# Kernel optimization log

Hardware: AMD Instinct MI355X
Metric: run time of the kernel (lower is better)

## Reference

```python
import jax, jax.numpy as jnp
import numpy as np

B, T, D = 2, 2048, 1024
H, RANK = 16, 32
DH = D // H  # 64


def setup_inputs() -> dict:
    key = jax.random.key(0)
    ks = jax.random.split(key, 6)
    sd = 1.0 / np.sqrt(D)
    sdh = 1.0 / np.sqrt(DH)
    return {
        "x": jax.random.normal(ks[0], (B, T, D), dtype=jnp.float32),
        "W_qkv": jax.random.normal(ks[1], (D, 3 * D), dtype=jnp.float32) * sd,
        "W_q_lsr": jax.random.normal(ks[2], (H, DH, RANK), dtype=jnp.float32) * sdh,
        "W_k_lsr": jax.random.normal(ks[3], (H, DH, RANK), dtype=jnp.float32) * sdh,
        "lsr_core": jnp.ones((H, RANK), dtype=jnp.float32),
        "W_o": jax.random.normal(ks[4], (D, D), dtype=jnp.float32) * sd,
    }


def reference(x, W_qkv, W_q_lsr, W_k_lsr, lsr_core, W_o):
    b, t, d = x.shape
    # Fused QKV projection
    qkv = x @ W_qkv  # (B, T, 3D)
    q, k, v = jnp.split(qkv, 3, axis=-1)
    # (B, H, T, DH)
    q = q.reshape(b, t, H, DH).transpose(0, 2, 1, 3)
    k = k.reshape(b, t, H, DH).transpose(0, 2, 1, 3)
    v = v.reshape(b, t, H, DH).transpose(0, 2, 1, 3)
    # Low-rank bilinear score: q^T Wq diag(core) Wk^T k
    ql = jnp.einsum("bhtd,hdr->bhtr", q, W_q_lsr)  # (B, H, T, R)
    kl = jnp.einsum("bhsd,hdr->bhsr", k, W_k_lsr)  # (B, H, T, R)
    scale = 1.0 / jnp.sqrt(jnp.asarray(RANK, dtype=x.dtype))
    scores = jnp.einsum("bhtr,bhsr->bhts", ql * lsr_core[None, :, None, :], kl) * scale
    # Causal mask
    causal = jnp.tril(jnp.ones((t, t), dtype=bool))
    scores = jnp.where(causal[None, None], scores, jnp.asarray(-jnp.inf, dtype=scores.dtype))
    attn = jax.nn.softmax(scores, axis=-1)
    y = jnp.einsum("bhts,bhsd->bhtd", attn, v)  # (B, H, T, DH)
    y = y.transpose(0, 2, 1, 3).reshape(b, t, d)
    return y @ W_o
```

## Files before the change

### kernel.cpp

```cpp
#include <hip/hip_runtime.h>
#include <hip/hip_bf16.h>

#define B_  2
#define T_  2048
#define D_  1024
#define H_  16
#define DH_ 64
#define R_  32
#define BT_ (B_*T_)
#define BH_ (B_*H_)

typedef unsigned short u16;
typedef unsigned int   u32;
typedef __attribute__((ext_vector_type(8))) short bhalf8;
typedef __attribute__((ext_vector_type(4))) float floatx4;

#define WSB_FLAG  0
#define WSB_XB    256
#define WSB_WCATT (WSB_XB    + 8388608)
#define WSB_QL    (WSB_WCATT + 4194304)
#define WSB_KL    (WSB_QL    + 4194304)
#define WSB_VT    (WSB_KL    + 4194304)
#define WSB_YB    (WSB_VT    + 8388608)
#define WSB_WOT   (WSB_YB    + 8388608)

#define NEG_ -1.0e30f

__device__ __forceinline__ float bfs(u16 s) {
    union { u32 i; float f; } w; w.i = ((u32)s) << 16; return w.f;
}
__device__ __forceinline__ u16 tob(float f) {
    __hip_bfloat16 h = __float2bfloat16(f);
    return *(u16*)&h;
}
__device__ __forceinline__ u32 pack2(float a, float b) {
    return (u32)tob(a) | ((u32)tob(b) << 16);
}

__global__ __launch_bounds__(64) void detect_dtype(const u32* __restrict__ xw,
                                                   int* __restrict__ flag)
{
    const int tid = threadIdx.x;
    int hits = 0;
    for (int i = tid; i < 512; i += 64) {
        const u32 w = xw[i];
        const u32 h = w & 0xFFFFu;
        const u32 e = (h >> 7) & 0xFFu;
        if (h == 0u || (e >= 100u && e <= 150u)) ++hits;
    }
    #pragma unroll
    for (int off = 32; off; off >>= 1) hits += __shfl_down(hits, off, 64);
    if (tid == 0) *flag = (hits >= 300) ? 1 : 0;
}

__global__ __launch_bounds__(256) void convert_x(
    const void* __restrict__ x, u16* __restrict__ xb,
    const int* __restrict__ flag)
{
    const int isbf = *flag;
    const int e = blockIdx.x * 256 + threadIdx.x;
    if (isbf) {
        ((uint4*)xb)[e] = ((const uint4*)x)[e];
    } else {
        float4 a0 = ((const float4*)x)[2*e];
        float4 a1 = ((const float4*)x)[2*e + 1];
        uint4 o;
        o.x = pack2(a0.x, a0.y); o.y = pack2(a0.z, a0.w);
        o.z = pack2(a1.x, a1.y); o.w = pack2(a1.z, a1.w);
        ((uint4*)xb)[e] = o;
    }
}

__global__ __launch_bounds__(256) void fold_mfma(
    const void* __restrict__ Wqkv, const void* __restrict__ Wq_lsr,
    const void* __restrict__ Wk_lsr, const void* __restrict__ core,
    u16* __restrict__ WcatT, const int* __restrict__ flag)
{
    __shared__ __align__(16) u16 Bq[128 * 72];
    __shared__ __align__(16) u16 Bk[128 * 72];
    __shared__ __align__(16) u16 Aq[32 * 72];
    __shared__ __align__(16) u16 Ak[32 * 72];
    const int isbf = *flag;
    const int tid  = threadIdx.x;
    const int lane = tid & 63;
    const int w    = tid >> 6;
    const int n16  = lane & 15;
    const int q4   = lane >> 4;
    const int h    = blockIdx.y;
    const int d0   = blockIdx.x * 128;

    #pragma unroll
    for (int p = 0; p < 8; ++p) {
        const int e  = tid + p * 256;
        const int r  = e & 31, dh = e >> 5;
        float aq, ak;
        if (isbf) {
            aq = bfs(((const u16*)Wq_lsr)[(h*DH_ + dh)*R_ + r]);
            ak = bfs(((const u16*)Wk_lsr)[(h*DH_ + dh)*R_ + r]);
        } else {
            aq = ((const float*)Wq_lsr)[(h*DH_ + dh)*R_ + r];
            ak = ((const float*)Wk_lsr)[(h*DH_ + dh)*R_ + r];
        }
        Aq[r * 72 + dh] = tob(aq);
        Ak[r * 72 + dh] = tob(ak);
    }
    #pragma unroll
    for (int p = 0; p < 8; ++p) {
        const int e  = tid + p * 256;
        const int n  = e >> 4, ch = e & 15;
        if (isbf) {
            uint2 wq = *(const uint2*)((const u16*)Wqkv + (size_t)(d0+n)*(3*D_) + h*DH_ + ch*4);
            uint2 wk = *(const uint2*)((const u16*)Wqkv + (size_t)(d0+n)*(3*D_) + D_ + h*DH_ + ch*4);
            *(uint2*)&Bq[n * 72 + ch*4] = wq;
            *(uint2*)&Bk[n * 72 + ch*4] = wk;
        } else {
            float4 fq = *(const float4*)((const float*)Wqkv + (size_t)(d0+n)*(3*D_) + h*DH_ + ch*4);
            float4 fk = *(const float4*)((const float*)Wqkv + (size_t)(d0+n)*(3*D_) + D_ + h*DH_ + ch*4);
            uint2 oq, ok;
            oq.x = pack2(fq.x, fq.y); oq.y = pack2(fq.z, fq.w);
            ok.x = pack2(fk.x, fk.y); ok.y = pack2(fk.z, fk.w);
            *(uint2*)&Bq[n * 72 + ch*4] = oq;
            *(uint2*)&Bk[n * 72 + ch*4] = ok;
        }
    }
    __syncthreads();

    floatx4 accq[2][2], acck[2][2];
    #pragma unroll
    for (int mi = 0; mi < 2; ++mi)
        #pragma unroll
        for (int ni = 0; ni < 2; ++ni) { accq[mi][ni] = (floatx4)(0.f); acck[mi][ni] = (floatx4)(0.f); }

    #pragma unroll
    for (int kk = 0; kk < 2; ++kk) {
        bhalf8 aqf[2], akf[2], bqf[2], bkf[2];
        #pragma unroll
        for (int mi = 0; mi < 2; ++mi) {
            aqf[mi] = *(const bhalf8*)&Aq[(mi*16 + n16) * 72 + kk*32 + q4*8];
            akf[mi] = *(const bhalf8*)&Ak[(mi*16 + n16) * 72 + kk*32 + q4*8];
        }
        #pragma unroll
        for (int ni = 0; ni < 2; ++ni) {
            bqf[ni] = *(const bhalf8*)&Bq[(w*32 + ni*16 + n16) * 72 + kk*32 + q4*8];
            bkf[ni] = *(const bhalf8*)&Bk[(w*32 + ni*16 + n16) * 72 + kk*32 + q4*8];
        }
        #pragma unroll
        for (int mi = 0; mi < 2; ++mi)
            #pragma unroll
            for (int ni = 0; ni < 2; ++ni) {
                accq[mi][ni] = __builtin_amdgcn_mfma_f32_16x16x32_bf16(aqf[mi], bqf[ni], accq[mi][ni], 0, 0, 0);
                acck[mi][ni] = __builtin_amdgcn_mfma_f32_16x16x32_bf16(akf[mi], bkf[ni], acck[mi][ni], 0, 0, 0);
            }
    }

    const float scale = 0.17677669529663687f;
    #pragma unroll
    for (int mi = 0; mi < 2; ++mi) {
        #pragma unroll
        for (int rr = 0; rr < 4; ++rr) {
            const int r = mi*16 + q4*4 + rr;
            const float cc = (isbf ? bfs(((const u16*)core)[h*R_ + r])
                                   : ((const float*)core)[h*R_ + r]) * scale;
            #pragma unroll
            for (int ni = 0; ni < 2; ++ni) {
                const int d = d0 + w*32 + ni*16 + n16;
                WcatT[(size_t)(h*R_ + r) * D_ + d]       = tob(accq[mi][ni][rr] * cc);
                WcatT[(size_t)(512 + h*R_ + r) * D_ + d] = tob(acck[mi][ni][rr]);
            }
        }
    }
}

__global__ __launch_bounds__(256) void convert_T(
    const void* __restrict__ src, u16* __restrict__ dst,
    int srcStride, int srcColOff, int dstRowOff, const int* __restrict__ flag)
{
    __shared__ __align__(16) u16 tile[64 * 72];
    const int isbf = *flag;
    const int tid = threadIdx.x;
    const int j0  = blockIdx.x * 64;
    const int i0  = blockIdx.y * 64;
    #pragma unroll
    for (int p = 0; p < 2; ++p) {
        const int e = tid + p * 256;
        const int r = e >> 3, ch = e & 7;
        if (isbf) {
            uint4 w = *(const uint4*)((const u16*)src + (size_t)(i0 + r) * srcStride + srcColOff + j0 + ch*8);
            *(uint4*)&tile[r * 72 + ch*8] = w;
        } else {
            const float* s = (const float*)src + (size_t)(i0 + r) * srcStride + srcColOff + j0 + ch*8;
            float4 a0 = *(const float4*)s;
            float4 a1 = *(const float4*)(s + 4);
            uint4 o;
            o.x = pack2(a0.x, a0.y); o.y = pack2(a0.z, a0.w);
            o.z = pack2(a1.x, a1.y); o.w = pack2(a1.z, a1.w);
            *(uint4*)&tile[r * 72 + ch*8] = o;
        }
    }
    __syncthreads();
    #pragma unroll
    for (int p = 0; p < 2; ++p) {
        const int e = tid + p * 256;
        const int c = e >> 3, ch = e & 7;
        u16 tmp[8];
        #pragma unroll
        for (int j = 0; j < 8; ++j) tmp[j] = tile[(ch*8 + j) * 72 + c];
        *(uint4*)(dst + (size_t)(dstRowOff + j0 + c) * D_ + i0 + ch*8) = *(uint4*)tmp;
    }
}

__global__ __launch_bounds__(256) void gemm1_mfma(
    const u16* __restrict__ xb, const u16* __restrict__ WcatT,
    u16* __restrict__ ql, u16* __restrict__ kl, u16* __restrict__ v_t)
{
    __shared__ __align__(16) u16 As[128 * 72];
    __shared__ __align__(16) u16 Bs[64 * 72];
    const int tid  = threadIdx.x;
    const int lane = tid & 63;
    const int w    = tid >> 6;
    const int n16  = lane & 15;
    const int q4   = lane >> 4;
    const int wx   = w & 1;
    const int wy   = w >> 1;
    const int bm   = blockIdx.y * 128;
    const int bn   = blockIdx.x * 64;

    floatx4 acc[4][2];
    #pragma unroll
    for (int i = 0; i < 4; ++i)
        #pragma unroll
        for (int j = 0; j < 2; ++j) acc[i][j] = (floatx4)(0.f);

    for (int kt = 0; kt < D_; kt += 64) {
        #pragma unroll
        for (int p = 0; p < 4; ++p) {
            const int e = tid + p * 256;
            const int r = e >> 3, ch = (e & 7) * 8;
            *(uint4*)&As[r * 72 + ch] = *(const uint4*)(xb + (size_t)(bm + r) * D_ + kt + ch);
        }
        #pragma unroll
        for (int p = 0; p < 2; ++p) {
            const int e = tid + p * 256;
            const int r = e >> 3, ch = (e & 7) * 8;
            *(uint4*)&Bs[r * 72 + ch] = *(const uint4*)(WcatT + (size_t)(bn + r) * D_ + kt + ch);
        }
        __syncthreads();
        #pragma unroll
        for (int kk = 0; kk < 2; ++kk) {
            bhalf8 a[4], b[2];
            #pragma unroll
            for (int mi = 0; mi < 4; ++mi)
                a[mi] = *(const bhalf8*)&As[(wy*64 + mi*16 + n16) * 72 + kk*32 + q4*8];
            #pragma unroll
            for (int ni = 0; ni < 2; ++ni)
                b[ni] = *(const bhalf8*)&Bs[(wx*32 + ni*16 + n16) * 72 + kk*32 + q4*8];
            #pragma unroll
            for (int mi = 0; mi < 4; ++mi)
                #pragma unroll
                for (int ni = 0; ni < 2; ++ni)
                    acc[mi][ni] = __builtin_amdgcn_mfma_f32_16x16x32_bf16(
                        a[mi], b[ni], acc[mi][ni], 0, 0, 0);
        }
        __syncthreads();
    }

    if (bn < 1024) {
        #pragma unroll
        for (int mi = 0; mi < 4; ++mi) {
            #pragma unroll
            for (int rr = 0; rr < 4; ++rr) {
                const int row = bm + wy*64 + mi*16 + q4*4 + rr;
                const int b   = row >> 11;
                const int t   = row & (T_ - 1);
                #pragma unroll
                for (int ni = 0; ni < 2; ++ni) {
                    const int col = bn + wx*32 + ni*16 + n16;
                    const u16 val = tob(acc[mi][ni][rr]);
                    if (col < 512) {
                        const int h = col >> 5, r = col & 31;
                        ql[((size_t)(b*H_ + h)*T_ + t)*R_ + r] = val;
                    } else {
                        const int c = col - 512; const int h = c >> 5, r = c & 31;
                        kl[((size_t)(b*H_ + h)*T_ + t)*R_ + r] = val;
                    }
                }
            }
        }
    } else {
        #pragma unroll
        for (int mi = 0; mi < 4; ++mi) {
            const int row0 = bm + wy*64 + mi*16 + q4*4;
            const int b = row0 >> 11;
            const int t = row0 & (T_ - 1);
            #pragma unroll
            for (int ni = 0; ni < 2; ++ni) {
                const int c = bn - 1024 + wx*32 + ni*16 + n16;
                const int h = c >> 6, dh = c & 63;
                uint2 o;
                o.x = pack2(acc[mi][ni][0], acc[mi][ni][1]);
                o.y = pack2(acc[mi][ni][2], acc[mi][ni][3]);
                *(uint2*)(v_t + ((size_t)(b*H_ + h) * DH_ + dh) * T_ + t) = o;
            }
        }
    }
}

__global__ __launch_bounds__(256, 2) void attn_kernel(
    const u16* __restrict__ ql, const u16* __restrict__ kl,
    const u16* __restrict__ v_t, u16* __restrict__ y)
{
    __shared__ __align__(16) u16 qls[64 * 40];
    __shared__ __align__(16) u16 kls[128 * 40];
    __shared__ __align__(16) u16 vsT[64 * 136];
    __shared__ __align__(16) u16 Ps [64 * 144];

    const int tid  = threadIdx.x;
    const int lane = tid & 63;
    const int w    = tid >> 6;
    const int n16  = lane & 15;
    const int q4   = lane >> 4;
    const int bh   = blockIdx.x;
    const int qt   = 31 - (int)blockIdx.y;
    const int t0   = qt * 64;
    const int nt   = (qt + 2) >> 1;

    {
        const int r = tid >> 2, ch = tid & 3;
        uint4 x = *(const uint4*)(ql + ((size_t)bh * T_ + t0 + r) * R_ + ch*8);
        *(uint4*)&qls[r * 40 + ch*8] = x;
    }
    bhalf8 aq = *(const bhalf8*)&qls[(w*16 + n16) * 40 + q4*8];

    const u16* klb = kl  + (size_t)bh * T_ * R_;
    const u16* vtb = v_t + (size_t)bh * DH_ * T_;
    const int rk = tid >> 2, ck = (tid & 3) * 8;
    const int dv = tid >> 4, cv = (tid & 15) * 8;

    uint4 kc0 = *(const uint4*)(klb + (size_t)(rk     ) * R_ + ck);
    uint4 kc1 = *(const uint4*)(klb + (size_t)(rk + 64) * R_ + ck);
    uint4 vc0 = *(const uint4*)(vtb + (size_t)(dv     ) * T_ + cv);
    uint4 vc1 = *(const uint4*)(vtb + (size_t)(dv + 16) * T_ + cv);
    uint4 vc2 = *(const uint4*)(vtb + (size_t)(dv + 32) * T_ + cv);
    uint4 vc3 = *(const uint4*)(vtb + (size_t)(dv + 48) * T_ + cv);
    uint4 kn0 = kc0, kn1 = kc1, vn0 = vc0, vn1 = vc1, vn2 = vc2, vn3 = vc3;

    float m[4], l[4];
    floatx4 O[4];
    #pragma unroll
    for (int r = 0; r < 4; ++r) { m[r] = NEG_; l[r] = 0.f; }
    #pragma unroll
    for (int c = 0; c < 4; ++c) O[c] = (floatx4)(0.f);

    for (int it = 0; it < nt; ++it) {
        const int s0 = it * 128;
        __syncthreads();
        *(uint4*)&kls[(rk     ) * 40 + ck] = kc0;
        *(uint4*)&kls[(rk + 64) * 40 + ck] = kc1;
        *(uint4*)&vsT[(dv     ) * 136 + cv] = vc0;
        *(uint4*)&vsT[(dv + 16) * 136 + cv] = vc1;
        *(uint4*)&vsT[(dv + 32) * 136 + cv] = vc2;
        *(uint4*)&vsT[(dv + 48) * 136 + cv] = vc3;
        if (it + 1 < nt) {
            const int s1 = s0 + 128;
            kn0 = *(const uint4*)(klb + (size_t)(s1 + rk     ) * R_ + ck);
            kn1 = *(const uint4*)(klb + (size_t)(s1 + rk + 64) * R_ + ck);
            vn0 = *(const uint4*)(vtb + (size_t)(dv     ) * T_ + s1 + cv);
            vn1 = *(const uint4*)(vtb + (size_t)(dv + 16) * T_ + s1 + cv);
            vn2 = *(const uint4*)(vtb + (size_t)(dv + 32) * T_ + s1 + cv);
            vn3 = *(const uint4*)(vtb + (size_t)(dv + 48) * T_ + s1 + cv);
        }
        __syncthreads();

        floatx4 Sc[8];
        #pragma unroll
        for (int c = 0; c < 8; ++c) {
            bhalf8 bk = *(const bhalf8*)&kls[(16*c + n16) * 40 + q4*8];
            Sc[c] = __builtin_amdgcn_mfma_f32_16x16x32_bf16(aq, bk, (floatx4)(0.f), 0, 0, 0);
        }

        if (it == nt - 1) {
            const int tg = t0 + w*16 + q4*4;
            #pragma unroll
            for (int c = 0; c < 8; ++c) {
                const int sg = s0 + 16*c + n16;
                #pragma unroll
                for (int r = 0; r < 4; ++r)
                    if (sg > tg + r) Sc[c][r] = NEG_;
            }
        }

        float rmax[4];
        #pragma unroll
        for (int r = 0; r < 4; ++r) {
            float a0 = fmaxf(fmaxf(Sc[0][r], Sc[1][r]), fmaxf(Sc[2][r], Sc[3][r]));
            float a1 = fmaxf(fmaxf(Sc[4][r], Sc[5][r]), fmaxf(Sc[6][r], Sc[7][r]));
            rmax[r] = fmaxf(a0, a1);
        }
        #pragma unroll
        for (int off = 1; off <= 8; off <<= 1)
            #pragma unroll
            for (int r = 0; r < 4; ++r)
                rmax[r] = fmaxf(rmax[r], __shfl_xor(rmax[r], off, 64));

        float alpha[4], rsum[4];
        #pragma unroll
        for (int r = 0; r < 4; ++r) {
            const float mn = fmaxf(m[r], rmax[r]);
            alpha[r] = __expf(m[r] - mn);
            m[r] = mn;
            rsum[r] = 0.f;
        }
        #pragma unroll
        for (int c = 0; c < 8; ++c)
            #pragma unroll
            for (int r = 0; r < 4; ++r) {
                const float p = __expf(Sc[c][r] - m[r]);
                Sc[c][r] = p;
                rsum[r] += p;
            }
        #pragma unroll
        for (int off = 1; off <= 8; off <<= 1)
            #pragma unroll
            for (int r = 0; r < 4; ++r)
                rsum[r] += __shfl_xor(rsum[r], off, 64);
        #pragma unroll
        for (int r = 0; r < 4; ++r) l[r] = l[r] * alpha[r] + rsum[r];
        #pragma unroll
        for (int c = 0; c < 4; ++c)
            #pragma unroll
            for (int r = 0; r < 4; ++r)
                O[c][r] *= alpha[r];

        #pragma unroll
        for (int c = 0; c < 8; ++c)
            #pragma unroll
            for (int r = 0; r < 4; ++r)
                Ps[(w*16 + r*4 + q4) * 144 + 16*c + n16] = tob(Sc[c][r]);

        const int slot = w*16 + (n16 & 3)*4 + (n16 >> 2);
        #pragma unroll
        for (int kc = 0; kc < 4; ++kc) {
            bhalf8 pa = *(const bhalf8*)&Ps[slot * 144 + kc*32 + q4*8];
            #pragma unroll
            for (int c2 = 0; c2 < 4; ++c2) {
                bhalf8 bv = *(const bhalf8*)&vsT[(16*c2 + n16) * 136 + kc*32 + q4*8];
                O[c2] = __builtin_amdgcn_mfma_f32_16x16x32_bf16(pa, bv, O[c2], 0, 0, 0);
            }
        }

        kc0 = kn0; kc1 = kn1; vc0 = vn0; vc1 = vn1; vc2 = vn2; vc3 = vn3;
    }

    const int b = bh >> 4, h = bh & 15;
    #pragma unroll
    for (int r = 0; r < 4; ++r) {
        const float rl = 1.0f / l[r];
        const int t = t0 + w*16 + q4*4 + r;
        #pragma unroll
        for (int c2 = 0; c2 < 4; ++c2)
            y[((size_t)b * T_ + t) * D_ + h * DH_ + 16*c2 + n16] = tob(O[c2][r] * rl);
    }
}

__global__ __launch_bounds__(256) void out_gemm_mfma(
    const u16* __restrict__ yb, const u16* __restrict__ WoT,
    float* __restrict__ out)
{
    __shared__ __align__(16) u16 As[128 * 72];
    __shared__ __align__(16) u16 Bs[64 * 72];
    const int tid  = threadIdx.x;
    const int lane = tid & 63;
    const int w    = tid >> 6;
    const int n16  = lane & 15;
    const int q4   = lane >> 4;
    const int wx   = w & 1;
    const int wy   = w >> 1;
    const int bm   = blockIdx.y * 128;
    const int bn   = blockIdx.x * 64;

    floatx4 acc[4][2];
    #pragma unroll
    for (int i = 0; i < 4; ++i)
        #pragma unroll
        for (int j = 0; j < 2; ++j) acc[i][j] = (floatx4)(0.f);

    for (int kt = 0; kt < D_; kt += 64) {
        #pragma unroll
        for (int p = 0; p < 4; ++p) {
            const int e = tid + p * 256;
            const int r = e >> 3, ch = (e & 7) * 8;
            *(uint4*)&As[r * 72 + ch] = *(const uint4*)(yb + (size_t)(bm + r) * D_ + kt + ch);
        }
        #pragma unroll
        for (int p = 0; p < 2; ++p) {
            const int e = tid + p * 256;
            const int r = e >> 3, ch = (e & 7) * 8;
            *(uint4*)&Bs[r * 72 + ch] = *(const uint4*)(WoT + (size_t)(bn + r) * D_ + kt + ch);
        }
        __syncthreads();
        #pragma unroll
        for (int kk = 0; kk < 2; ++kk) {
            bhalf8 a[4], b[2];
            #pragma unroll
            for (int mi = 0; mi < 4; ++mi)
                a[mi] = *(const bhalf8*)&As[(wy*64 + mi*16 + n16) * 72 + kk*32 + q4*8];
            #pragma unroll
            for (int ni = 0; ni < 2; ++ni)
                b[ni] = *(const bhalf8*)&Bs[(wx*32 + ni*16 + n16) * 72 + kk*32 + q4*8];
            #pragma unroll
            for (int mi = 0; mi < 4; ++mi)
                #pragma unroll
                for (int ni = 0; ni < 2; ++ni)
                    acc[mi][ni] = __builtin_amdgcn_mfma_f32_16x16x32_bf16(
                        a[mi], b[ni], acc[mi][ni], 0, 0, 0);
        }
        __syncthreads();
    }

    #pragma unroll
    for (int mi = 0; mi < 4; ++mi) {
        #pragma unroll
        for (int rr = 0; rr < 4; ++rr) {
            const int row = bm + wy*64 + mi*16 + q4*4 + rr;
            #pragma unroll
            for (int ni = 0; ni < 2; ++ni) {
                const int col = bn + wx*32 + ni*16 + n16;
                out[(size_t)row * D_ + col] = acc[mi][ni][rr];
            }
        }
    }
}

extern "C" void kernel_launch(void* const* d_in, const int* in_sizes, int n_in,
                              void* d_out, int out_size, void* d_ws, size_t ws_size,
                              hipStream_t stream)
{
    (void)out_size; (void)ws_size;
    const void* in_x = nullptr; const void* in_wqkv = nullptr;
    const void* in_wq = nullptr; const void* in_wk = nullptr;
    const void* in_core = nullptr; const void* in_wo = nullptr;
    for (int i = 0; i < n_in; ++i) {
        const int s = in_sizes[i];
        if      (s == BT_*D_)     { if (!in_x)    in_x    = d_in[i]; }
        else if (s == D_*3*D_)    { if (!in_wqkv) in_wqkv = d_in[i]; }
        else if (s == H_*DH_*R_)  { if (!in_wq)   in_wq   = d_in[i]; else if (!in_wk) in_wk = d_in[i]; }
        else if (s == H_*R_)      { if (!in_core) in_core = d_in[i]; }
        else if (s == D_*D_)      { if (!in_wo)   in_wo   = d_in[i]; }
    }
    if (!in_x)    in_x    = d_in[0];
    if (!in_wqkv) in_wqkv = d_in[1];
    if (!in_wq)   in_wq   = d_in[2];
    if (!in_wk)   in_wk   = d_in[3];
    if (!in_core) in_core = d_in[4];
    if (!in_wo)   in_wo   = d_in[5];

    float* out = (float*)d_out;

    char* ws    = (char*)d_ws;
    int*  flag  = (int*)(ws + WSB_FLAG);
    u16*  xb    = (u16*)(ws + WSB_XB);
    u16*  WcatT = (u16*)(ws + WSB_WCATT);
    u16*  ql    = (u16*)(ws + WSB_QL);
    u16*  kl    = (u16*)(ws + WSB_KL);
    u16*  v_t   = (u16*)(ws + WSB_VT);
    u16*  yb    = (u16*)(ws + WSB_YB);
    u16*  WoT   = (u16*)(ws + WSB_WOT);

    detect_dtype<<<1, 64, 0, stream>>>((const u32*)in_x, flag);
    convert_x<<<2048, 256, 0, stream>>>(in_x, xb, flag);
    fold_mfma<<<dim3(8, 16), 256, 0, stream>>>(in_wqkv, in_wq, in_wk, in_core, WcatT, flag);
    convert_T<<<dim3(16,16), 256, 0, stream>>>(in_wqkv, WcatT, 3*D_, 2*D_, 1024, flag);
    convert_T<<<dim3(16,16), 256, 0, stream>>>(in_wo,   WoT,   D_,   0,    0,    flag);
    gemm1_mfma<<<dim3(32, 32), 256, 0, stream>>>(xb, WcatT, ql, kl, v_t);
    attn_kernel<<<dim3(32, 32), 256, 0, stream>>>(ql, kl, v_t, yb);
    out_gemm_mfma<<<dim3(16, 32), 256, 0, stream>>>(yb, WoT, out);
}
```

Measured before the change: 196.2 us.

## Transpose score MFMA so softmax rows are lane-local, use exp2 and skip rescale

The score MFMA operands are swapped so each lane holds one query row across keys, which turns the row max and sum into in-register reductions plus two cross-lane shuffles. log2(e) is folded into the Wq scale so the softmax can use the exp2 intrinsic directly, and the O rescale is skipped when no row maximum grows anywhere in the wave. The Q shared-memory staging is dropped, P is written in packed 8-byte stores, and launch bounds ask for three blocks per CU. The alpha and l values need extra shuffles to reach the O layout, and the higher occupancy target may increase register pressure or cause spills.

```diff
diff --git a/kernel.cpp b/kernel.cpp
--- a/kernel.cpp
+++ b/kernel.cpp
@@ -153,7 +153,7 @@
             }
     }
 
-    const float scale = 0.17677669529663687f;
+    const float scale = (float)(0.17677669529663687 * 1.4426950408889634);
     #pragma unroll
     for (int mi = 0; mi < 2; ++mi) {
         #pragma unroll
@@ -305,14 +305,13 @@
     }
 }
 
-__global__ __launch_bounds__(256, 2) void attn_kernel(
+__global__ __launch_bounds__(256, 3) void attn_kernel(
     const u16* __restrict__ ql, const u16* __restrict__ kl,
     const u16* __restrict__ v_t, u16* __restrict__ y)
 {
-    __shared__ __align__(16) u16 qls[64 * 40];
     __shared__ __align__(16) u16 kls[128 * 40];
     __shared__ __align__(16) u16 vsT[64 * 136];
-    __shared__ __align__(16) u16 Ps [64 * 144];
+    __shared__ __align__(16) u16 Ps [4][16][144];
 
     const int tid  = threadIdx.x;
     const int lane = tid & 63;
@@ -324,12 +323,8 @@
     const int t0   = qt * 64;
     const int nt   = (qt + 2) >> 1;
 
-    {
-        const int r = tid >> 2, ch = tid & 3;
-        uint4 x = *(const uint4*)(ql + ((size_t)bh * T_ + t0 + r) * R_ + ch*8);
-        *(uint4*)&qls[r * 40 + ch*8] = x;
-    }
-    bhalf8 aq = *(const bhalf8*)&qls[(w*16 + n16) * 40 + q4*8];
+    const u16* qlb = ql + (size_t)bh * T_ * R_;
+    const bhalf8 aq = *(const bhalf8*)(qlb + (size_t)(t0 + w*16 + n16) * R_ + q4*8);
 
     const u16* klb = kl  + (size_t)bh * T_ * R_;
     const u16* vtb = v_t + (size_t)bh * DH_ * T_;
@@ -344,10 +339,8 @@
     uint4 vc3 = *(const uint4*)(vtb + (size_t)(dv + 48) * T_ + cv);
     uint4 kn0 = kc0, kn1 = kc1, vn0 = vc0, vn1 = vc1, vn2 = vc2, vn3 = vc3;
 
-    float m[4], l[4];
+    float mrow = NEG_, lrow = 0.f;
     floatx4 O[4];
-    #pragma unroll
-    for (int r = 0; r < 4; ++r) { m[r] = NEG_; l[r] = 0.f; }
     #pragma unroll
     for (int c = 0; c < 4; ++c) O[c] = (floatx4)(0.f);
 
@@ -374,73 +367,72 @@
         floatx4 Sc[8];
         #pragma unroll
         for (int c = 0; c < 8; ++c) {
-            bhalf8 bk = *(const bhalf8*)&kls[(16*c + n16) * 40 + q4*8];
-            Sc[c] = __builtin_amdgcn_mfma_f32_16x16x32_bf16(aq, bk, (floatx4)(0.f), 0, 0, 0);
+            bhalf8 ak = *(const bhalf8*)&kls[(16*c + n16) * 40 + q4*8];
+            Sc[c] = __builtin_amdgcn_mfma_f32_16x16x32_bf16(ak, aq, (floatx4)(0.f), 0, 0, 0);
         }
 
         if (it == nt - 1) {
-            const int tg = t0 + w*16 + q4*4;
+            const int tq = w*16 + n16;
             #pragma unroll
             for (int c = 0; c < 8; ++c) {
-                const int sg = s0 + 16*c + n16;
+                const int sb = s0 - t0 + 16*c + 4*q4;
                 #pragma unroll
                 for (int r = 0; r < 4; ++r)
-                    if (sg > tg + r) Sc[c][r] = NEG_;
-            }
-        }
-
-        float rmax[4];
-        #pragma unroll
-        for (int r = 0; r < 4; ++r) {
-            float a0 = fmaxf(fmaxf(Sc[0][r], Sc[1][r]), fmaxf(Sc[2][r], Sc[3][r]));
-            float a1 = fmaxf(fmaxf(Sc[4][r], Sc[5][r]), fmaxf(Sc[6][r], Sc[7][r]));
-            rmax[r] = fmaxf(a0, a1);
-        }
-        #pragma unroll
-        for (int off = 1; off <= 8; off <<= 1)
+                    if (sb + r > tq) Sc[c][r] = NEG_;
+            }
+        }
+
+        float cmax[8];
+        #pragma unroll
+        for (int c = 0; c < 8; ++c)
+            cmax[c] = fmaxf(fmaxf(Sc[c][0], Sc[c][1]), fmaxf(Sc[c][2], Sc[c][3]));
+        float rmax = fmaxf(fmaxf(fmaxf(cmax[0], cmax[1]), fmaxf(cmax[2], cmax[3])),
+                           fmaxf(fmaxf(cmax[4], cmax[5]), fmaxf(cmax[6], cmax[7])));
+        rmax = fmaxf(rmax, __shfl_xor(rmax, 16, 64));
+        rmax = fmaxf(rmax, __shfl_xor(rmax, 32, 64));
+
+        const float mn = fmaxf(mrow, rmax);
+        const int norescale = __all(rmax <= mrow);
+
+        float csum[8];
+        #pragma unroll
+        for (int c = 0; c < 8; ++c) {
             #pragma unroll
             for (int r = 0; r < 4; ++r)
-                rmax[r] = fmaxf(rmax[r], __shfl_xor(rmax[r], off, 64));
-
-        float alpha[4], rsum[4];
-        #pragma unroll
-        for (int r = 0; r < 4; ++r) {
-            const float mn = fmaxf(m[r], rmax[r]);
-            alpha[r] = __expf(m[r] - mn);
-            m[r] = mn;
-            rsum[r] = 0.f;
-        }
-        #pragma unroll
-        for (int c = 0; c < 8; ++c)
-            #pragma unroll
-            for (int r = 0; r < 4; ++r) {
-                const float p = __expf(Sc[c][r] - m[r]);
-                Sc[c][r] = p;
-                rsum[r] += p;
-            }
-        #pragma unroll
-        for (int off = 1; off <= 8; off <<= 1)
-            #pragma unroll
-            for (int r = 0; r < 4; ++r)
-                rsum[r] += __shfl_xor(rsum[r], off, 64);
-        #pragma unroll
-        for (int r = 0; r < 4; ++r) l[r] = l[r] * alpha[r] + rsum[r];
-        #pragma unroll
-        for (int c = 0; c < 4; ++c)
-            #pragma unroll
-            for (int r = 0; r < 4; ++r)
-                O[c][r] *= alpha[r];
-
-        #pragma unroll
-        for (int c = 0; c < 8; ++c)
-            #pragma unroll
-            for (int r = 0; r < 4; ++r)
-                Ps[(w*16 + r*4 + q4) * 144 + 16*c + n16] = tob(Sc[c][r]);
-
-        const int slot = w*16 + (n16 & 3)*4 + (n16 >> 2);
+                Sc[c][r] = __builtin_amdgcn_exp2f(Sc[c][r] - mn);
+            csum[c] = (Sc[c][0] + Sc[c][1]) + (Sc[c][2] + Sc[c][3]);
+        }
+        float rsum = ((csum[0] + csum[1]) + (csum[2] + csum[3]))
+                   + ((csum[4] + csum[5]) + (csum[6] + csum[7]));
+        rsum += __shfl_xor(rsum, 16, 64);
+        rsum += __shfl_xor(rsum, 32, 64);
+
+        if (norescale) {
+            lrow += rsum;
+        } else {
+            const float alpha = __builtin_amdgcn_exp2f(mrow - mn);
+            mrow = mn;
+            lrow = lrow * alpha + rsum;
+            float aO[4];
+            #pragma unroll
+            for (int r = 0; r < 4; ++r) aO[r] = __shfl(alpha, q4*4 + r, 64);
+            #pragma unroll
+            for (int c2 = 0; c2 < 4; ++c2)
+                #pragma unroll
+                for (int r = 0; r < 4; ++r) O[c2][r] *= aO[r];
+        }
+
+        #pragma unroll
+        for (int c = 0; c < 8; ++c) {
+            uint2 pw;
+            pw.x = pack2(Sc[c][0], Sc[c][1]);
+            pw.y = pack2(Sc[c][2], Sc[c][3]);
+            *(uint2*)&Ps[w][n16][16*c + 4*q4] = pw;
+        }
+
         #pragma unroll
         for (int kc = 0; kc < 4; ++kc) {
-            bhalf8 pa = *(const bhalf8*)&Ps[slot * 144 + kc*32 + q4*8];
+            bhalf8 pa = *(const bhalf8*)&Ps[w][n16][kc*32 + q4*8];
             #pragma unroll
             for (int c2 = 0; c2 < 4; ++c2) {
                 bhalf8 bv = *(const bhalf8*)&vsT[(16*c2 + n16) * 136 + kc*32 + q4*8];
@@ -452,9 +444,12 @@
     }
 
     const int b = bh >> 4, h = bh & 15;
+    float lb[4];
+    #pragma unroll
+    for (int r = 0; r < 4; ++r) lb[r] = __shfl(lrow, q4*4 + r, 64);
     #pragma unroll
     for (int r = 0; r < 4; ++r) {
-        const float rl = 1.0f / l[r];
+        const float rl = 1.0f / lb[r];
         const int t = t0 + w*16 + q4*4 + r;
         #pragma unroll
         for (int c2 = 0; c2 < 4; ++c2)
```

Measured after the change: 189.0 us. 3.6% less time.
